# Performance work log

Measured on AMD Instinct MI355X. Metric: run time of the kernel, lower is better.

Reference implementation:

```python
import jax, jax.numpy as jnp
import numpy as np

B, L, D = 4, 4096, 256


def setup_inputs() -> dict:
    key = jax.random.key(0)
    k_x, k_q, k_k, k_v, k_w, k_b = jax.random.split(key, 6)
    s = 1.0 / np.sqrt(D)
    return {
        "x": jax.random.normal(k_x, (B, L, D), dtype=jnp.float32),
        "Wq": jax.random.normal(k_q, (D, D), dtype=jnp.float32) * s,   # nn.Linear weight (out,in)
        "Wk": jax.random.normal(k_k, (D, D), dtype=jnp.float32) * s,
        "Wv": jax.random.normal(k_v, (D, D), dtype=jnp.float32) * s,
        "w_mlp": jax.random.normal(k_w, (D,), dtype=jnp.float32) * s,  # Linear(D,1) weight
        "b_mlp": jnp.zeros((), dtype=jnp.float32),                     # Linear(D,1) bias
    }


def reference(x, Wq, Wk, Wv, w_mlp, b_mlp):
    # Projections (nn.Linear: y = x @ W.T, no bias)
    Q = jnp.einsum("bld,ed->ble", x, Wq)
    K = jnp.einsum("bld,ed->ble", x, Wk)
    V = jnp.einsum("bld,ed->ble", x, Wv)
    # score[b,i,j] = relu((Q[b,i]-K[b,j]) @ w_mlp + b_mlp)
    # decomposed: (Q-K)@w = Q@w - K@w  (exact same math, no (B,L,L,D) tensor)
    q_s = Q @ w_mlp  # (B,L)
    k_s = K @ w_mlp  # (B,L)
    scores = jax.nn.relu(q_s[:, :, None] - k_s[:, None, :] + b_mlp)  # (B,L,L)
    attn = jax.nn.softmax(scores, axis=-1)  # softmax over key axis j
    # out[b,i,d] = sum_j attn[b,i,j] * V[b,j,d]
    out = jnp.einsum("bij,bjd->bid", attn, V)
    return out  # dropout p=0.0 is identity
```

## Files before the change

kernel.cpp:

```cpp
#include <hip/hip_runtime.h>
#include <math.h>

#define BB 4
#define LL 4096
#define DD 256
#define NROWS (BB*LL)
#define CHUNK 32
#define NC (LL/CHUNK)
#define NB 8192

typedef __bf16 bf16x8 __attribute__((ext_vector_type(8)));
typedef __bf16 bf16x4 __attribute__((ext_vector_type(4)));
typedef float floatx4 __attribute__((ext_vector_type(4)));

__global__ void k_prep(const float* __restrict__ Wq, const float* __restrict__ Wk,
                       const float* __restrict__ Wv, const float* __restrict__ w,
                       float* __restrict__ u_part,
                       __bf16* __restrict__ Wh, __bf16* __restrict__ Wl) {
    __shared__ float wl[16];
    int d = threadIdx.x;
    int e0 = blockIdx.x * 16;
    if (d < 16) wl[d] = w[e0 + d];
    __syncthreads();
    float aq = 0.f, ak = 0.f;
    #pragma unroll
    for (int j = 0; j < 16; ++j) {
        float we = wl[j];
        aq = fmaf(Wq[(size_t)(e0 + j)*DD + d], we, aq);
        ak = fmaf(Wk[(size_t)(e0 + j)*DD + d], we, ak);
        float wv = Wv[(size_t)(e0 + j)*DD + d];
        __bf16 h = (__bf16)wv;
        Wh[(size_t)(e0 + j)*DD + d] = h;
        Wl[(size_t)(e0 + j)*DD + d] = (__bf16)(wv - (float)h);
    }
    u_part[(size_t)blockIdx.x*512 + d]       = aq;
    u_part[(size_t)blockIdx.x*512 + DD + d]  = ak;
}

__global__ void __launch_bounds__(256) k_gemm_mfma(
        const float* __restrict__ x,
        const __bf16* __restrict__ Wh, const __bf16* __restrict__ Wl,
        const float* __restrict__ u_part, const float* __restrict__ bmlp,
        float* __restrict__ V, float* __restrict__ a, float* __restrict__ c) {
    __shared__ __bf16 Ah[2][32*40];
    __shared__ __bf16 Al[2][32*40];
    __shared__ float4 ul[128];
    __shared__ float pros[512];
    const int tid = threadIdx.x;
    const int wave = tid >> 6, lane = tid & 63;
    const int rowBase = blockIdx.x * 32;
    const int colBase = blockIdx.y * 128;
    const int quad = lane >> 4, l16 = lane & 15;
    const int srow = tid >> 3, skq = (tid & 7) * 4;
    const bool doproj = (blockIdx.y == 0);

    if (doproj && tid < 128) {
        float4 s = make_float4(0.f, 0.f, 0.f, 0.f);
        #pragma unroll
        for (int g = 0; g < 16; ++g) {
            float4 p = *(const float4*)(u_part + (size_t)g*512 + tid*4);
            s.x += p.x; s.y += p.y; s.z += p.z; s.w += p.w;
        }
        ul[tid] = s;
    }
    __syncthreads();

    floatx4 acc[2][2];
    #pragma unroll
    for (int rt = 0; rt < 2; ++rt)
        #pragma unroll
        for (int ct = 0; ct < 2; ++ct)
            acc[rt][ct] = (floatx4){0.f, 0.f, 0.f, 0.f};
    float aq = 0.f, ak = 0.f;

    const float* xrow = x + (size_t)(rowBase + srow)*DD + skq;

    {
        float4 xv = *(const float4*)xrow;
        __bf16 h0 = (__bf16)xv.x, h1 = (__bf16)xv.y, h2 = (__bf16)xv.z, h3 = (__bf16)xv.w;
        bf16x4 hv = {h0, h1, h2, h3};
        bf16x4 lv = {(__bf16)(xv.x - (float)h0), (__bf16)(xv.y - (float)h1),
                     (__bf16)(xv.z - (float)h2), (__bf16)(xv.w - (float)h3)};
        *(bf16x4*)&Ah[0][srow*40 + skq] = hv;
        *(bf16x4*)&Al[0][srow*40 + skq] = lv;
        if (doproj) {
            float4 q4 = ul[(tid & 7)];
            float4 k4 = ul[64 + (tid & 7)];
            aq = fmaf(xv.x, q4.x, fmaf(xv.y, q4.y, fmaf(xv.z, q4.z, fmaf(xv.w, q4.w, aq))));
            ak = fmaf(xv.x, k4.x, fmaf(xv.y, k4.y, fmaf(xv.z, k4.z, fmaf(xv.w, k4.w, ak))));
        }
    }
    __syncthreads();

    for (int t = 0; t < 8; ++t) {
        const int k0 = t * 32;
        const int cur = t & 1;
        float4 xv;
        if (t < 7) xv = *(const float4*)(xrow + k0 + 32);
        bf16x8 ah[2], al[2];
        #pragma unroll
        for (int rt = 0; rt < 2; ++rt) {
            int m = rt*16 + l16;
            ah[rt] = *(bf16x8*)&Ah[cur][m*40 + quad*8];
            al[rt] = *(bf16x8*)&Al[cur][m*40 + quad*8];
        }
        if (t < 7) {
            __bf16 h0 = (__bf16)xv.x, h1 = (__bf16)xv.y, h2 = (__bf16)xv.z, h3 = (__bf16)xv.w;
            bf16x4 hv = {h0, h1, h2, h3};
            bf16x4 lv = {(__bf16)(xv.x - (float)h0), (__bf16)(xv.y - (float)h1),
                         (__bf16)(xv.z - (float)h2), (__bf16)(xv.w - (float)h3)};
            *(bf16x4*)&Ah[cur^1][srow*40 + skq] = hv;
            *(bf16x4*)&Al[cur^1][srow*40 + skq] = lv;
            if (doproj) {
                float4 q4 = ul[((k0 + 32) >> 2) + (tid & 7)];
                float4 k4 = ul[64 + ((k0 + 32) >> 2) + (tid & 7)];
                aq = fmaf(xv.x, q4.x, fmaf(xv.y, q4.y, fmaf(xv.z, q4.z, fmaf(xv.w, q4.w, aq))));
                ak = fmaf(xv.x, k4.x, fmaf(xv.y, k4.y, fmaf(xv.z, k4.z, fmaf(xv.w, k4.w, ak))));
            }
        }
        __syncthreads();
        #pragma unroll
        for (int ct = 0; ct < 2; ++ct) {
            int n = colBase + wave*32 + ct*16 + l16;
            bf16x8 bh = *(const bf16x8*)(Wh + (size_t)n*DD + k0 + quad*8);
            bf16x8 bl = *(const bf16x8*)(Wl + (size_t)n*DD + k0 + quad*8);
            #pragma unroll
            for (int rt = 0; rt < 2; ++rt) {
                acc[rt][ct] = __builtin_amdgcn_mfma_f32_16x16x32_bf16(ah[rt], bh, acc[rt][ct], 0, 0, 0);
                acc[rt][ct] = __builtin_amdgcn_mfma_f32_16x16x32_bf16(ah[rt], bl, acc[rt][ct], 0, 0, 0);
                acc[rt][ct] = __builtin_amdgcn_mfma_f32_16x16x32_bf16(al[rt], bh, acc[rt][ct], 0, 0, 0);
            }
        }
    }
    #pragma unroll
    for (int rt = 0; rt < 2; ++rt)
        #pragma unroll
        for (int ct = 0; ct < 2; ++ct)
            #pragma unroll
            for (int i = 0; i < 4; ++i) {
                int row = rowBase + rt*16 + quad*4 + i;
                int col = colBase + wave*32 + ct*16 + l16;
                V[(size_t)row*DD + col] = acc[rt][ct][i];
            }
    if (doproj) {
        __syncthreads();
        pros[tid] = aq;
        pros[256 + tid] = ak;
        __syncthreads();
        if (tid < 32) {
            float sa = 0.f, sc = 0.f;
            #pragma unroll
            for (int j = 0; j < 8; ++j) {
                sa += pros[tid*8 + j];
                sc += pros[256 + tid*8 + j];
            }
            a[rowBase + tid] = sa + bmlp[0];
            c[rowBase + tid] = sc;
        }
    }
}

__global__ void __launch_bounds__(1024) k_sortish(const float* __restrict__ c,
        int* __restrict__ binstart_g, int* __restrict__ perm,
        float* __restrict__ c_sorted, float* __restrict__ e_sorted,
        float* __restrict__ SE, float* __restrict__ hdr) {
    __shared__ int   hist[NB];
    __shared__ float esl[LL];
    __shared__ float scrf[64];
    int b = blockIdx.x, tid = threadIdx.x;
    int wave = tid >> 6, lane = tid & 63;
    int* scri = (int*)scrf;

    float4 cv = ((const float4*)(c + (size_t)b*LL))[tid];
    float cw[4] = {cv.x, cv.y, cv.z, cv.w};
    float mn = fminf(fminf(cw[0],cw[1]), fminf(cw[2],cw[3]));
    float mx = fmaxf(fmaxf(cw[0],cw[1]), fmaxf(cw[2],cw[3]));
    #pragma unroll
    for (int off = 32; off > 0; off >>= 1) {
        mn = fminf(mn, __shfl_down(mn, off));
        mx = fmaxf(mx, __shfl_down(mx, off));
    }
    if (lane == 0) { scrf[wave] = mn; scrf[32 + wave] = mx; }
    __syncthreads();
    if (wave == 0) {
        float m = (lane < 16) ? scrf[lane]      :  3.4e38f;
        float M = (lane < 16) ? scrf[32 + lane] : -3.4e38f;
        #pragma unroll
        for (int off = 32; off > 0; off >>= 1) {
            m = fminf(m, __shfl_down(m, off));
            M = fmaxf(M, __shfl_down(M, off));
        }
        if (lane == 0) { scrf[0] = m; scrf[1] = M; }
    }
    __syncthreads();
    float cmin = scrf[0], cmax = scrf[1];
    float scale = (float)NB / fmaxf(cmax - cmin, 1e-20f);
    __syncthreads();

    ((int4*)hist)[tid] = make_int4(0,0,0,0);
    ((int4*)hist)[tid + 1024] = make_int4(0,0,0,0);
    __syncthreads();

    int bins[4];
    #pragma unroll
    for (int u = 0; u < 4; ++u) {
        int bi = (int)((cw[u] - cmin) * scale);
        bi = bi < 0 ? 0 : (bi > NB-1 ? NB-1 : bi);
        bins[u] = bi;
        atomicAdd(&hist[bi], 1);
    }
    __syncthreads();

    int loc[8]; int base = 0;
    #pragma unroll
    for (int j = 0; j < 8; ++j) { loc[j] = base; base += hist[tid*8 + j]; }
    int incl = base;
    #pragma unroll
    for (int off = 1; off < 64; off <<= 1) {
        int t = __shfl_up(incl, off);
        if (lane >= off) incl += t;
    }
    if (lane == 63) scri[wave] = incl;
    __syncthreads();
    if (wave == 0) {
        int v = (lane < 16) ? scri[lane] : 0;
        int s = v;
        #pragma unroll
        for (int off = 1; off < 16; off <<= 1) {
            int t = __shfl_up(s, off);
            if (lane >= off) s += t;
        }
        if (lane < 16) scri[lane] = s - v;
    }
    __syncthreads();
    int thread_excl = (incl - base) + scri[wave];
    __syncthreads();
    #pragma unroll
    for (int j = 0; j < 8; ++j) {
        int bs = thread_excl + loc[j];
        binstart_g[(size_t)b*(NB+2) + tid*8 + j] = bs;
        hist[tid*8 + j] = bs;
    }
    if (tid == 0) {
        binstart_g[(size_t)b*(NB+2) + NB]     = LL;
        binstart_g[(size_t)b*(NB+2) + NB + 1] = LL;
        hdr[b*2 + 0] = cmin;
        hdr[b*2 + 1] = scale;
    }
    __syncthreads();

    #pragma unroll
    for (int u = 0; u < 4; ++u) {
        int i = tid*4 + u;
        int r = atomicAdd(&hist[bins[u]], 1);
        float e = expf(cmin - cw[u]);
        perm[(size_t)b*LL + r] = i;
        c_sorted[(size_t)b*LL + r] = cw[u];
        e_sorted[(size_t)b*LL + r] = e;
        esl[r] = e;
    }
    __syncthreads();

    float le[4]; float s0 = 0.f;
    #pragma unroll
    for (int u = 0; u < 4; ++u) { le[u] = s0; s0 += esl[tid*4 + u]; }
    float fincl = s0;
    #pragma unroll
    for (int off = 1; off < 64; off <<= 1) {
        float t = __shfl_up(fincl, off);
        if (lane >= off) fincl += t;
    }
    if (lane == 63) scrf[wave] = fincl;
    __syncthreads();
    if (wave == 0) {
        float v = (lane < 16) ? scrf[lane] : 0.f;
        float s = v;
        #pragma unroll
        for (int off = 1; off < 16; off <<= 1) {
            float t = __shfl_up(s, off);
            if (lane >= off) s += t;
        }
        if (lane < 16) scrf[lane] = s - v;
    }
    __syncthreads();
    float texcl = (fincl - s0) + scrf[wave];
    #pragma unroll
    for (int u = 0; u < 4; ++u)
        SE[(size_t)b*(LL+1) + tid*4 + u] = texcl + le[u];
    if (tid == 1023) SE[(size_t)b*(LL+1) + LL] = texcl + s0;
}

__global__ void k_scan(const float* __restrict__ V, const int* __restrict__ perm,
        const float* __restrict__ e_sorted,
        float* __restrict__ Pl, float* __restrict__ Pel,
        float* __restrict__ Tp, float* __restrict__ Te) {
    int b = blockIdx.y, q = blockIdx.x;
    int d = threadIdx.x;
    __shared__ int pj[CHUNK];
    __shared__ float pe[CHUNK];
    if (d < CHUNK) {
        pj[d] = perm[(size_t)b*LL + q*CHUNK + d];
        pe[d] = e_sorted[(size_t)b*LL + q*CHUNK + d];
    }
    __syncthreads();
    float vr[CHUNK];
    #pragma unroll
    for (int r = 0; r < CHUNK; ++r)
        vr[r] = V[((size_t)b*LL + pj[r]) * DD + d];
    float acc = 0.f, acce = 0.f;
    size_t kb = (size_t)b*LL + (size_t)q*CHUNK;
    #pragma unroll
    for (int r = 0; r < CHUNK; ++r) {
        size_t o = (kb + r) * DD + d;
        Pl[o]  = acc;
        Pel[o] = acce;
        acc += vr[r];
        acce = fmaf(pe[r], vr[r], acce);
    }
    size_t to = ((size_t)b*NC + q) * DD + d;
    Tp[to] = acc;
    Te[to] = acce;
}

__global__ void k_base(const float* __restrict__ Tp, const float* __restrict__ Te,
        float* __restrict__ baseP, float* __restrict__ basePe) {
    int q = blockIdx.x, b = blockIdx.y, d = threadIdx.x;
    float acc = 0.f, acce = 0.f;
    #pragma unroll 8
    for (int i = 0; i < q; ++i) {
        size_t ti = ((size_t)b*NC + i) * DD + d;
        acc += Tp[ti]; acce += Te[ti];
    }
    size_t o = ((size_t)b*(NC+1) + q) * DD + d;
    baseP[o] = acc; basePe[o] = acce;
}

__global__ void k_out(const float* __restrict__ a, const float* __restrict__ hdr,
                      const int* __restrict__ binstart,
                      const float* __restrict__ c_sorted, const float* __restrict__ e_sorted,
                      const int* __restrict__ perm, const float* __restrict__ V,
                      const float* __restrict__ SE,
                      const float* __restrict__ Pl, const float* __restrict__ Pel,
                      const float* __restrict__ baseP, const float* __restrict__ basePe,
                      float* __restrict__ out) {
    int row = blockIdx.x * 4 + (threadIdx.x >> 6);
    int lane = threadIdx.x & 63;
    int b = row >> 12;
    float ai = a[row];
    float cmin = hdr[b*2 + 0], scale = hdr[b*2 + 1];
    float t = (ai - cmin) * scale;
    int ib = t < 0.f ? 0 : (t >= (float)NB ? NB : (int)t);
    int k    = binstart[(size_t)b*(NB+2) + ib];
    int kend = binstart[(size_t)b*(NB+2) + ib + 1];
    float alpha = expf(cmin - ai);
    float Z = fmaf(alpha, (float)(LL - k), SE[(size_t)b*(LL+1) + k]);
    size_t db = (size_t)lane * 4;
    size_t totoff = ((size_t)b * (NC+1) + NC) * DD + db;
    float4 ptot  = *(const float4*)(baseP  + totoff);
    float4 pk, pek;
    if (k < LL) {
        int q = k >> 5;
        size_t po = ((size_t)b * LL + k) * DD + db;
        size_t bo = ((size_t)b * (NC+1) + q) * DD + db;
        float4 pl = *(const float4*)(Pl    + po);
        float4 bp = *(const float4*)(baseP + bo);
        float4 pe = *(const float4*)(Pel    + po);
        float4 be = *(const float4*)(basePe + bo);
        pk.x = pl.x + bp.x; pk.y = pl.y + bp.y; pk.z = pl.z + bp.z; pk.w = pl.w + bp.w;
        pek.x = pe.x + be.x; pek.y = pe.y + be.y; pek.z = pe.z + be.z; pek.w = pe.w + be.w;
    } else {
        pk = ptot;
        pek = *(const float4*)(basePe + totoff);
    }
    float4 num;
    num.x = fmaf(alpha, ptot.x - pk.x, pek.x);
    num.y = fmaf(alpha, ptot.y - pk.y, pek.y);
    num.z = fmaf(alpha, ptot.z - pk.z, pek.z);
    num.w = fmaf(alpha, ptot.w - pk.w, pek.w);
    for (int r = k; r < kend; ++r) {
        float cr = c_sorted[(size_t)b*LL + r];
        if (cr < ai) {
            float w = e_sorted[(size_t)b*LL + r] - alpha;
            int j = perm[(size_t)b*LL + r];
            float4 v = *(const float4*)(V + ((size_t)b*LL + j) * DD + db);
            num.x = fmaf(w, v.x, num.x);
            num.y = fmaf(w, v.y, num.y);
            num.z = fmaf(w, v.z, num.z);
            num.w = fmaf(w, v.w, num.w);
            Z += w;
        }
    }
    float invZ = 1.f / Z;
    float4 o;
    o.x = num.x * invZ; o.y = num.y * invZ; o.z = num.z * invZ; o.w = num.w * invZ;
    *(float4*)(out + (size_t)row * DD + db) = o;
}

extern "C" void kernel_launch(void* const* d_in, const int* in_sizes, int n_in,
                              void* d_out, int out_size, void* d_ws, size_t ws_size,
                              hipStream_t stream) {
    const float* x  = (const float*)d_in[0];
    const float* Wq = (const float*)d_in[1];
    const float* Wk = (const float*)d_in[2];
    const float* Wv = (const float*)d_in[3];
    const float* wm = (const float*)d_in[4];
    const float* bm = (const float*)d_in[5];
    float* out = (float*)d_out;
    float* ws = (float*)d_ws;

    size_t off = 0;
    auto alloc = [&](size_t n) {
        float* p = ws + off;
        off += (n + 255) & ~(size_t)255;
        return p;
    };
    float* u_part   = alloc(16*512);
    float* a        = alloc(NROWS);
    float* c        = alloc(NROWS);
    float* c_sorted = alloc(NROWS);
    float* e_sorted = alloc(NROWS);
    float* SE       = alloc((size_t)BB*(LL+1));
    int*   perm     = (int*)alloc(NROWS);
    int*   binstart = (int*)alloc((size_t)BB*(NB+2));
    float* hdr      = alloc(2*BB);
    float* V        = alloc((size_t)NROWS*DD);
    float* Pl       = alloc((size_t)NROWS*DD);
    float* Pel      = alloc((size_t)NROWS*DD);
    float* Tp       = alloc((size_t)BB*NC*DD);
    float* Te       = alloc((size_t)BB*NC*DD);
    float* baseP    = alloc((size_t)BB*(NC+1)*DD);
    float* basePe   = alloc((size_t)BB*(NC+1)*DD);
    __bf16* Wh      = (__bf16*)alloc((size_t)DD*DD/2);
    __bf16* Wl      = (__bf16*)alloc((size_t)DD*DD/2);

    hipLaunchKernelGGL(k_prep, dim3(16), dim3(DD), 0, stream, Wq, Wk, Wv, wm, u_part, Wh, Wl);
    hipLaunchKernelGGL(k_gemm_mfma, dim3(NROWS/32, 2), dim3(256), 0, stream,
                       x, Wh, Wl, u_part, bm, V, a, c);
    hipLaunchKernelGGL(k_sortish, dim3(BB), dim3(1024), 0, stream,
                       c, binstart, perm, c_sorted, e_sorted, SE, hdr);
    hipLaunchKernelGGL(k_scan, dim3(NC, BB), dim3(DD), 0, stream, V, perm, e_sorted, Pl, Pel, Tp, Te);
    hipLaunchKernelGGL(k_base, dim3(NC+1, BB), dim3(DD), 0, stream, Tp, Te, baseP, basePe);
    hipLaunchKernelGGL(k_out, dim3(NROWS/4), dim3(256), 0, stream,
                       a, hdr, binstart, c_sorted, e_sorted, perm, V,
                       SE, Pl, Pel, baseP, basePe, out);
}
```

Baseline: 135.1 us.

## Replace bucket sort with exact rank-by-counting and fuse scan stages

Replaces the single-block-per-batch histogram bucket sort with an exact parallel rank kernel. Each key, packed as an order-preserving float encoding with its index, counts how many keys are smaller. Query rows get their exact insertion rank the same way, so the per-row in-bin correction loop in the output kernel goes away. The per-batch min is now computed with atomics inside the GEMM epilogue, and the SE prefix scan is merged into the chunk-scan kernel, which uses 1024-thread blocks. The trade-off is quadratic comparison work (about 4096x8192 per batch) in exchange for far more parallelism and one fewer serial kernel.

```diff
diff --git a/kernel.cpp b/kernel.cpp
--- a/kernel.cpp
+++ b/kernel.cpp
@@ -7,19 +7,29 @@
 #define NROWS (BB*LL)
 #define CHUNK 32
 #define NC (LL/CHUNK)
-#define NB 8192
 
 typedef __bf16 bf16x8 __attribute__((ext_vector_type(8)));
 typedef __bf16 bf16x4 __attribute__((ext_vector_type(4)));
 typedef float floatx4 __attribute__((ext_vector_type(4)));
+typedef unsigned long long u64;
+
+__device__ __forceinline__ unsigned encf(float f) {
+    unsigned u = __float_as_uint(f);
+    return (u & 0x80000000u) ? ~u : (u | 0x80000000u);
+}
+__device__ __forceinline__ float decf(unsigned u) {
+    return __uint_as_float((u & 0x80000000u) ? (u ^ 0x80000000u) : ~u);
+}
 
 __global__ void k_prep(const float* __restrict__ Wq, const float* __restrict__ Wk,
                        const float* __restrict__ Wv, const float* __restrict__ w,
                        float* __restrict__ u_part,
-                       __bf16* __restrict__ Wh, __bf16* __restrict__ Wl) {
+                       __bf16* __restrict__ Wh, __bf16* __restrict__ Wl,
+                       unsigned* __restrict__ hdru) {
     __shared__ float wl[16];
     int d = threadIdx.x;
     int e0 = blockIdx.x * 16;
+    if (blockIdx.x == 0 && d < 8) hdru[d] = (d & 1) ? 0u : 0xFFFFFFFFu;
     if (d < 16) wl[d] = w[e0 + d];
     __syncthreads();
     float aq = 0.f, ak = 0.f;
@@ -41,7 +51,9 @@
         const float* __restrict__ x,
         const __bf16* __restrict__ Wh, const __bf16* __restrict__ Wl,
         const float* __restrict__ u_part, const float* __restrict__ bmlp,
-        float* __restrict__ V, float* __restrict__ a, float* __restrict__ c) {
+        float* __restrict__ V, float* __restrict__ a,
+        u64* __restrict__ ckeys, u64* __restrict__ akeys,
+        unsigned* __restrict__ hdru) {
     __shared__ __bf16 Ah[2][32*40];
     __shared__ __bf16 Al[2][32*40];
     __shared__ float4 ul[128];
@@ -154,172 +166,129 @@
                 sa += pros[tid*8 + j];
                 sc += pros[256 + tid*8 + j];
             }
-            a[rowBase + tid] = sa + bmlp[0];
-            c[rowBase + tid] = sc;
-        }
-    }
-}
-
-__global__ void __launch_bounds__(1024) k_sortish(const float* __restrict__ c,
-        int* __restrict__ binstart_g, int* __restrict__ perm,
-        float* __restrict__ c_sorted, float* __restrict__ e_sorted,
-        float* __restrict__ SE, float* __restrict__ hdr) {
-    __shared__ int   hist[NB];
-    __shared__ float esl[LL];
+            int grow = rowBase + tid;
+            float av = sa + bmlp[0];
+            a[grow] = av;
+            ckeys[grow] = ((u64)encf(sc) << 32) | (unsigned)(grow & (LL-1));
+            akeys[grow] = ((u64)encf(av) << 32);
+            float mn = sc, mx = sc;
+            #pragma unroll
+            for (int off = 16; off > 0; off >>= 1) {
+                mn = fminf(mn, __shfl_down(mn, off));
+                mx = fmaxf(mx, __shfl_down(mx, off));
+            }
+            if (tid == 0) {
+                int bb = rowBase >> 12;
+                atomicMin(&hdru[bb*2 + 0], encf(mn));
+                atomicMax(&hdru[bb*2 + 1], encf(mx));
+            }
+        }
+    }
+}
+
+__global__ void __launch_bounds__(256) k_rank(
+        const u64* __restrict__ ckeys, const u64* __restrict__ akeys,
+        const unsigned* __restrict__ hdru,
+        int* __restrict__ perm, float* __restrict__ e_sorted,
+        int* __restrict__ rowk)
+{
+    const int b = blockIdx.y, tid = threadIdx.x;
+    const int ql = tid >> 4, t = tid & 15;
+    const int g = blockIdx.x * 16 + ql;
+    const u64* kb = ckeys + (size_t)b*LL;
+    const u64 K = (g < LL) ? kb[g] : akeys[(size_t)b*LL + (g - LL)];
+    int cnt = 0;
+    #pragma unroll 16
+    for (int s = 0; s < 256; ++s) {
+        u64 km = kb[t + (s << 4)];
+        cnt += (km < K) ? 1 : 0;
+    }
+    cnt += __shfl_down(cnt, 8, 16);
+    cnt += __shfl_down(cnt, 4, 16);
+    cnt += __shfl_down(cnt, 2, 16);
+    cnt += __shfl_down(cnt, 1, 16);
+    if (t == 0) {
+        if (g < LL) {
+            float cj = decf((unsigned)(K >> 32));
+            float cmin = decf(hdru[b*2]);
+            perm[(size_t)b*LL + cnt] = g;
+            e_sorted[(size_t)b*LL + cnt] = expf(cmin - cj);
+        } else {
+            rowk[(size_t)b*LL + (g - LL)] = cnt;
+        }
+    }
+}
+
+__global__ void __launch_bounds__(1024) k_mid(
+        const int* __restrict__ perm, const float* __restrict__ e_sorted,
+        const float* __restrict__ V,
+        float* __restrict__ SE,
+        float* __restrict__ Pl, float* __restrict__ Pel,
+        float* __restrict__ Tp, float* __restrict__ Te)
+{
     __shared__ float scrf[64];
-    int b = blockIdx.x, tid = threadIdx.x;
-    int wave = tid >> 6, lane = tid & 63;
-    int* scri = (int*)scrf;
-
-    float4 cv = ((const float4*)(c + (size_t)b*LL))[tid];
-    float cw[4] = {cv.x, cv.y, cv.z, cv.w};
-    float mn = fminf(fminf(cw[0],cw[1]), fminf(cw[2],cw[3]));
-    float mx = fmaxf(fmaxf(cw[0],cw[1]), fmaxf(cw[2],cw[3]));
-    #pragma unroll
-    for (int off = 32; off > 0; off >>= 1) {
-        mn = fminf(mn, __shfl_down(mn, off));
-        mx = fmaxf(mx, __shfl_down(mx, off));
-    }
-    if (lane == 0) { scrf[wave] = mn; scrf[32 + wave] = mx; }
-    __syncthreads();
-    if (wave == 0) {
-        float m = (lane < 16) ? scrf[lane]      :  3.4e38f;
-        float M = (lane < 16) ? scrf[32 + lane] : -3.4e38f;
-        #pragma unroll
-        for (int off = 32; off > 0; off >>= 1) {
-            m = fminf(m, __shfl_down(m, off));
-            M = fmaxf(M, __shfl_down(M, off));
-        }
-        if (lane == 0) { scrf[0] = m; scrf[1] = M; }
-    }
-    __syncthreads();
-    float cmin = scrf[0], cmax = scrf[1];
-    float scale = (float)NB / fmaxf(cmax - cmin, 1e-20f);
-    __syncthreads();
-
-    ((int4*)hist)[tid] = make_int4(0,0,0,0);
-    ((int4*)hist)[tid + 1024] = make_int4(0,0,0,0);
-    __syncthreads();
-
-    int bins[4];
-    #pragma unroll
-    for (int u = 0; u < 4; ++u) {
-        int bi = (int)((cw[u] - cmin) * scale);
-        bi = bi < 0 ? 0 : (bi > NB-1 ? NB-1 : bi);
-        bins[u] = bi;
-        atomicAdd(&hist[bi], 1);
-    }
-    __syncthreads();
-
-    int loc[8]; int base = 0;
-    #pragma unroll
-    for (int j = 0; j < 8; ++j) { loc[j] = base; base += hist[tid*8 + j]; }
-    int incl = base;
-    #pragma unroll
-    for (int off = 1; off < 64; off <<= 1) {
-        int t = __shfl_up(incl, off);
-        if (lane >= off) incl += t;
-    }
-    if (lane == 63) scri[wave] = incl;
-    __syncthreads();
-    if (wave == 0) {
-        int v = (lane < 16) ? scri[lane] : 0;
-        int s = v;
-        #pragma unroll
-        for (int off = 1; off < 16; off <<= 1) {
-            int t = __shfl_up(s, off);
-            if (lane >= off) s += t;
-        }
-        if (lane < 16) scri[lane] = s - v;
-    }
-    __syncthreads();
-    int thread_excl = (incl - base) + scri[wave];
-    __syncthreads();
-    #pragma unroll
-    for (int j = 0; j < 8; ++j) {
-        int bs = thread_excl + loc[j];
-        binstart_g[(size_t)b*(NB+2) + tid*8 + j] = bs;
-        hist[tid*8 + j] = bs;
-    }
-    if (tid == 0) {
-        binstart_g[(size_t)b*(NB+2) + NB]     = LL;
-        binstart_g[(size_t)b*(NB+2) + NB + 1] = LL;
-        hdr[b*2 + 0] = cmin;
-        hdr[b*2 + 1] = scale;
-    }
-    __syncthreads();
-
-    #pragma unroll
-    for (int u = 0; u < 4; ++u) {
-        int i = tid*4 + u;
-        int r = atomicAdd(&hist[bins[u]], 1);
-        float e = expf(cmin - cw[u]);
-        perm[(size_t)b*LL + r] = i;
-        c_sorted[(size_t)b*LL + r] = cw[u];
-        e_sorted[(size_t)b*LL + r] = e;
-        esl[r] = e;
-    }
-    __syncthreads();
-
-    float le[4]; float s0 = 0.f;
-    #pragma unroll
-    for (int u = 0; u < 4; ++u) { le[u] = s0; s0 += esl[tid*4 + u]; }
-    float fincl = s0;
-    #pragma unroll
-    for (int off = 1; off < 64; off <<= 1) {
-        float t = __shfl_up(fincl, off);
-        if (lane >= off) fincl += t;
-    }
-    if (lane == 63) scrf[wave] = fincl;
-    __syncthreads();
-    if (wave == 0) {
-        float v = (lane < 16) ? scrf[lane] : 0.f;
-        float s = v;
-        #pragma unroll
-        for (int off = 1; off < 16; off <<= 1) {
-            float t = __shfl_up(s, off);
-            if (lane >= off) s += t;
-        }
-        if (lane < 16) scrf[lane] = s - v;
-    }
-    __syncthreads();
-    float texcl = (fincl - s0) + scrf[wave];
-    #pragma unroll
-    for (int u = 0; u < 4; ++u)
-        SE[(size_t)b*(LL+1) + tid*4 + u] = texcl + le[u];
-    if (tid == 1023) SE[(size_t)b*(LL+1) + LL] = texcl + s0;
-}
-
-__global__ void k_scan(const float* __restrict__ V, const int* __restrict__ perm,
-        const float* __restrict__ e_sorted,
-        float* __restrict__ Pl, float* __restrict__ Pel,
-        float* __restrict__ Tp, float* __restrict__ Te) {
-    int b = blockIdx.y, q = blockIdx.x;
-    int d = threadIdx.x;
-    __shared__ int pj[CHUNK];
-    __shared__ float pe[CHUNK];
-    if (d < CHUNK) {
-        pj[d] = perm[(size_t)b*LL + q*CHUNK + d];
-        pe[d] = e_sorted[(size_t)b*LL + q*CHUNK + d];
-    }
-    __syncthreads();
-    float vr[CHUNK];
-    #pragma unroll
-    for (int r = 0; r < CHUNK; ++r)
-        vr[r] = V[((size_t)b*LL + pj[r]) * DD + d];
-    float acc = 0.f, acce = 0.f;
-    size_t kb = (size_t)b*LL + (size_t)q*CHUNK;
-    #pragma unroll
-    for (int r = 0; r < CHUNK; ++r) {
-        size_t o = (kb + r) * DD + d;
-        Pl[o]  = acc;
-        Pel[o] = acce;
-        acc += vr[r];
-        acce = fmaf(pe[r], vr[r], acce);
-    }
-    size_t to = ((size_t)b*NC + q) * DD + d;
-    Tp[to] = acc;
-    Te[to] = acce;
+    __shared__ int   pj_l[4][CHUNK];
+    __shared__ float pe_l[4][CHUNK];
+    const int bid = blockIdx.x, tid = threadIdx.x;
+    if (bid < BB) {
+        const int b = bid, wave = tid >> 6, lane = tid & 63;
+        float4 ev = ((const float4*)(e_sorted + (size_t)b*LL))[tid];
+        float ew[4] = {ev.x, ev.y, ev.z, ev.w};
+        float le[4]; float s0 = 0.f;
+        #pragma unroll
+        for (int u = 0; u < 4; ++u) { le[u] = s0; s0 += ew[u]; }
+        float fincl = s0;
+        #pragma unroll
+        for (int off = 1; off < 64; off <<= 1) {
+            float tt = __shfl_up(fincl, off);
+            if (lane >= off) fincl += tt;
+        }
+        if (lane == 63) scrf[wave] = fincl;
+        __syncthreads();
+        if (wave == 0) {
+            float v = (lane < 16) ? scrf[lane] : 0.f;
+            float s = v;
+            #pragma unroll
+            for (int off = 1; off < 16; off <<= 1) {
+                float tt = __shfl_up(s, off);
+                if (lane >= off) s += tt;
+            }
+            if (lane < 16) scrf[lane] = s - v;
+        }
+        __syncthreads();
+        float texcl = (fincl - s0) + scrf[wave];
+        #pragma unroll
+        for (int u = 0; u < 4; ++u)
+            SE[(size_t)b*(LL+1) + tid*4 + u] = texcl + le[u];
+        if (tid == 1023) SE[(size_t)b*(LL+1) + LL] = texcl + s0;
+    } else {
+        const int task = bid - BB;
+        const int sub = tid >> 8, d = tid & 255;
+        const int chunk = task*4 + sub;
+        const int b = chunk >> 7, q = chunk & (NC-1);
+        if (d < CHUNK) {
+            pj_l[sub][d] = perm[(size_t)b*LL + q*CHUNK + d];
+            pe_l[sub][d] = e_sorted[(size_t)b*LL + q*CHUNK + d];
+        }
+        __syncthreads();
+        float vr[CHUNK];
+        #pragma unroll
+        for (int r = 0; r < CHUNK; ++r)
+            vr[r] = V[((size_t)b*LL + pj_l[sub][r])*DD + d];
+        float acc = 0.f, acce = 0.f;
+        size_t kb = (size_t)b*LL + (size_t)q*CHUNK;
+        #pragma unroll
+        for (int r = 0; r < CHUNK; ++r) {
+            size_t o = (kb + r)*DD + d;
+            Pl[o]  = acc;
+            Pel[o] = acce;
+            acc += vr[r];
+            acce = fmaf(pe_l[sub][r], vr[r], acce);
+        }
+        size_t to = ((size_t)b*NC + q)*DD + d;
+        Tp[to] = acc;
+        Te[to] = acce;
+    }
 }
 
 __global__ void k_base(const float* __restrict__ Tp, const float* __restrict__ Te,
@@ -335,10 +304,8 @@
     baseP[o] = acc; basePe[o] = acce;
 }
 
-__global__ void k_out(const float* __restrict__ a, const float* __restrict__ hdr,
-                      const int* __restrict__ binstart,
-                      const float* __restrict__ c_sorted, const float* __restrict__ e_sorted,
-                      const int* __restrict__ perm, const float* __restrict__ V,
+__global__ void k_out(const float* __restrict__ a, const unsigned* __restrict__ hdru,
+                      const int* __restrict__ rowk,
                       const float* __restrict__ SE,
                       const float* __restrict__ Pl, const float* __restrict__ Pel,
                       const float* __restrict__ baseP, const float* __restrict__ basePe,
@@ -347,16 +314,13 @@
     int lane = threadIdx.x & 63;
     int b = row >> 12;
     float ai = a[row];
-    float cmin = hdr[b*2 + 0], scale = hdr[b*2 + 1];
-    float t = (ai - cmin) * scale;
-    int ib = t < 0.f ? 0 : (t >= (float)NB ? NB : (int)t);
-    int k    = binstart[(size_t)b*(NB+2) + ib];
-    int kend = binstart[(size_t)b*(NB+2) + ib + 1];
+    float cmin = decf(hdru[b*2]);
+    int k = rowk[row];
     float alpha = expf(cmin - ai);
     float Z = fmaf(alpha, (float)(LL - k), SE[(size_t)b*(LL+1) + k]);
     size_t db = (size_t)lane * 4;
     size_t totoff = ((size_t)b * (NC+1) + NC) * DD + db;
-    float4 ptot  = *(const float4*)(baseP  + totoff);
+    float4 ptot = *(const float4*)(baseP + totoff);
     float4 pk, pek;
     if (k < LL) {
         int q = k >> 5;
@@ -377,19 +341,6 @@
     num.y = fmaf(alpha, ptot.y - pk.y, pek.y);
     num.z = fmaf(alpha, ptot.z - pk.z, pek.z);
     num.w = fmaf(alpha, ptot.w - pk.w, pek.w);
-    for (int r = k; r < kend; ++r) {
-        float cr = c_sorted[(size_t)b*LL + r];
-        if (cr < ai) {
-            float w = e_sorted[(size_t)b*LL + r] - alpha;
-            int j = perm[(size_t)b*LL + r];
-            float4 v = *(const float4*)(V + ((size_t)b*LL + j) * DD + db);
-            num.x = fmaf(w, v.x, num.x);
-            num.y = fmaf(w, v.y, num.y);
-            num.z = fmaf(w, v.z, num.z);
-            num.w = fmaf(w, v.w, num.w);
-            Z += w;
-        }
-    }
     float invZ = 1.f / Z;
     float4 o;
     o.x = num.x * invZ; o.y = num.y * invZ; o.z = num.z * invZ; o.w = num.w * invZ;
@@ -416,13 +367,11 @@
     };
     float* u_part   = alloc(16*512);
     float* a        = alloc(NROWS);
-    float* c        = alloc(NROWS);
-    float* c_sorted = alloc(NROWS);
     float* e_sorted = alloc(NROWS);
     float* SE       = alloc((size_t)BB*(LL+1));
     int*   perm     = (int*)alloc(NROWS);
-    int*   binstart = (int*)alloc((size_t)BB*(NB+2));
-    float* hdr      = alloc(2*BB);
+    int*   rowk     = (int*)alloc(NROWS);
+    unsigned* hdru  = (unsigned*)alloc(2*BB);
     float* V        = alloc((size_t)NROWS*DD);
     float* Pl       = alloc((size_t)NROWS*DD);
     float* Pel      = alloc((size_t)NROWS*DD);
@@ -430,17 +379,21 @@
     float* Te       = alloc((size_t)BB*NC*DD);
     float* baseP    = alloc((size_t)BB*(NC+1)*DD);
     float* basePe   = alloc((size_t)BB*(NC+1)*DD);
+    u64*   ckeys    = (u64*)alloc((size_t)NROWS*2);
+    u64*   akeys    = (u64*)alloc((size_t)NROWS*2);
     __bf16* Wh      = (__bf16*)alloc((size_t)DD*DD/2);
     __bf16* Wl      = (__bf16*)alloc((size_t)DD*DD/2);
 
-    hipLaunchKernelGGL(k_prep, dim3(16), dim3(DD), 0, stream, Wq, Wk, Wv, wm, u_part, Wh, Wl);
+    hipLaunchKernelGGL(k_prep, dim3(16), dim3(DD), 0, stream,
+                       Wq, Wk, Wv, wm, u_part, Wh, Wl, hdru);
     hipLaunchKernelGGL(k_gemm_mfma, dim3(NROWS/32, 2), dim3(256), 0, stream,
-                       x, Wh, Wl, u_part, bm, V, a, c);
-    hipLaunchKernelGGL(k_sortish, dim3(BB), dim3(1024), 0, stream,
-                       c, binstart, perm, c_sorted, e_sorted, SE, hdr);
-    hipLaunchKernelGGL(k_scan, dim3(NC, BB), dim3(DD), 0, stream, V, perm, e_sorted, Pl, Pel, Tp, Te);
-    hipLaunchKernelGGL(k_base, dim3(NC+1, BB), dim3(DD), 0, stream, Tp, Te, baseP, basePe);
+                       x, Wh, Wl, u_part, bm, V, a, ckeys, akeys, hdru);
+    hipLaunchKernelGGL(k_rank, dim3(512, BB), dim3(256), 0, stream,
+                       ckeys, akeys, hdru, perm, e_sorted, rowk);
+    hipLaunchKernelGGL(k_mid, dim3(BB + NC*BB/4), dim3(1024), 0, stream,
+                       perm, e_sorted, V, SE, Pl, Pel, Tp, Te);
+    hipLaunchKernelGGL(k_base, dim3(NC+1, BB), dim3(256), 0, stream,
+                       Tp, Te, baseP, basePe);
     hipLaunchKernelGGL(k_out, dim3(NROWS/4), dim3(256), 0, stream,
-                       a, hdr, binstart, c_sorted, e_sorted, perm, V,
-                       SE, Pl, Pel, baseP, basePe, out);
-}
+                       a, hdru, rowk, SE, Pl, Pel, baseP, basePe, out);
+}
```

Result: slower. 190.1 us (+40.7%).

## Move min/max into GEMM epilogue and prefix-sum of exp into scan kernel

Applied to the files above, without the earlier changes.

The per-batch min and max of c are now computed in the GEMM epilogue with wave shuffles plus order-preserving unsigned atomicMin/atomicMax, so the single-block-per-batch sort kernel no longer does its own two-level reduction. The exclusive prefix sum of the sorted exp weights (SE) is moved out of the sort kernel into one extra block per batch in the scan kernel. This shortens the serial, low-occupancy sort stage (only 4 blocks) at the cost of global atomics and an extra header initialisation in the prep kernel.

```diff
diff --git a/kernel.cpp b/kernel.cpp
--- a/kernel.cpp
+++ b/kernel.cpp
@@ -13,13 +13,23 @@
 typedef __bf16 bf16x4 __attribute__((ext_vector_type(4)));
 typedef float floatx4 __attribute__((ext_vector_type(4)));
 
+__device__ __forceinline__ unsigned encf(float f) {
+    unsigned u = __float_as_uint(f);
+    return (u & 0x80000000u) ? ~u : (u | 0x80000000u);
+}
+__device__ __forceinline__ float decf(unsigned u) {
+    return __uint_as_float((u & 0x80000000u) ? (u ^ 0x80000000u) : ~u);
+}
+
 __global__ void k_prep(const float* __restrict__ Wq, const float* __restrict__ Wk,
                        const float* __restrict__ Wv, const float* __restrict__ w,
                        float* __restrict__ u_part,
-                       __bf16* __restrict__ Wh, __bf16* __restrict__ Wl) {
+                       __bf16* __restrict__ Wh, __bf16* __restrict__ Wl,
+                       unsigned* __restrict__ hdru) {
     __shared__ float wl[16];
     int d = threadIdx.x;
     int e0 = blockIdx.x * 16;
+    if (blockIdx.x == 0 && d < 8) hdru[d] = (d & 1) ? 0u : 0xFFFFFFFFu;
     if (d < 16) wl[d] = w[e0 + d];
     __syncthreads();
     float aq = 0.f, ak = 0.f;
@@ -41,7 +51,8 @@
         const float* __restrict__ x,
         const __bf16* __restrict__ Wh, const __bf16* __restrict__ Wl,
         const float* __restrict__ u_part, const float* __restrict__ bmlp,
-        float* __restrict__ V, float* __restrict__ a, float* __restrict__ c) {
+        float* __restrict__ V, float* __restrict__ a, float* __restrict__ c,
+        unsigned* __restrict__ hdru) {
     __shared__ __bf16 Ah[2][32*40];
     __shared__ __bf16 Al[2][32*40];
     __shared__ float4 ul[128];
@@ -156,46 +167,36 @@
             }
             a[rowBase + tid] = sa + bmlp[0];
             c[rowBase + tid] = sc;
-        }
-    }
-}
-
-__global__ void __launch_bounds__(1024) k_sortish(const float* __restrict__ c,
+            float mn = sc, mx = sc;
+            #pragma unroll
+            for (int off = 16; off > 0; off >>= 1) {
+                mn = fminf(mn, __shfl_down(mn, off));
+                mx = fmaxf(mx, __shfl_down(mx, off));
+            }
+            if (tid == 0) {
+                int bb = rowBase >> 12;
+                atomicMin(&hdru[bb*2 + 0], encf(mn));
+                atomicMax(&hdru[bb*2 + 1], encf(mx));
+            }
+        }
+    }
+}
+
+__global__ void __launch_bounds__(1024) k_sortl(const float* __restrict__ c,
+        const unsigned* __restrict__ hdru,
         int* __restrict__ binstart_g, int* __restrict__ perm,
         float* __restrict__ c_sorted, float* __restrict__ e_sorted,
-        float* __restrict__ SE, float* __restrict__ hdr) {
-    __shared__ int   hist[NB];
-    __shared__ float esl[LL];
-    __shared__ float scrf[64];
+        float* __restrict__ hdrf) {
+    __shared__ int hist[NB];
+    __shared__ int scri[16];
     int b = blockIdx.x, tid = threadIdx.x;
     int wave = tid >> 6, lane = tid & 63;
-    int* scri = (int*)scrf;
 
     float4 cv = ((const float4*)(c + (size_t)b*LL))[tid];
     float cw[4] = {cv.x, cv.y, cv.z, cv.w};
-    float mn = fminf(fminf(cw[0],cw[1]), fminf(cw[2],cw[3]));
-    float mx = fmaxf(fmaxf(cw[0],cw[1]), fmaxf(cw[2],cw[3]));
-    #pragma unroll
-    for (int off = 32; off > 0; off >>= 1) {
-        mn = fminf(mn, __shfl_down(mn, off));
-        mx = fmaxf(mx, __shfl_down(mx, off));
-    }
-    if (lane == 0) { scrf[wave] = mn; scrf[32 + wave] = mx; }
-    __syncthreads();
-    if (wave == 0) {
-        float m = (lane < 16) ? scrf[lane]      :  3.4e38f;
-        float M = (lane < 16) ? scrf[32 + lane] : -3.4e38f;
-        #pragma unroll
-        for (int off = 32; off > 0; off >>= 1) {
-            m = fminf(m, __shfl_down(m, off));
-            M = fmaxf(M, __shfl_down(M, off));
-        }
-        if (lane == 0) { scrf[0] = m; scrf[1] = M; }
-    }
-    __syncthreads();
-    float cmin = scrf[0], cmax = scrf[1];
+    float cmin = decf(hdru[b*2 + 0]);
+    float cmax = decf(hdru[b*2 + 1]);
     float scale = (float)NB / fmaxf(cmax - cmin, 1e-20f);
-    __syncthreads();
 
     ((int4*)hist)[tid] = make_int4(0,0,0,0);
     ((int4*)hist)[tid + 1024] = make_int4(0,0,0,0);
@@ -244,8 +245,8 @@
     if (tid == 0) {
         binstart_g[(size_t)b*(NB+2) + NB]     = LL;
         binstart_g[(size_t)b*(NB+2) + NB + 1] = LL;
-        hdr[b*2 + 0] = cmin;
-        hdr[b*2 + 1] = scale;
+        hdrf[b*2 + 0] = cmin;
+        hdrf[b*2 + 1] = scale;
     }
     __syncthreads();
 
@@ -253,73 +254,81 @@
     for (int u = 0; u < 4; ++u) {
         int i = tid*4 + u;
         int r = atomicAdd(&hist[bins[u]], 1);
-        float e = expf(cmin - cw[u]);
         perm[(size_t)b*LL + r] = i;
         c_sorted[(size_t)b*LL + r] = cw[u];
-        e_sorted[(size_t)b*LL + r] = e;
-        esl[r] = e;
-    }
-    __syncthreads();
-
-    float le[4]; float s0 = 0.f;
-    #pragma unroll
-    for (int u = 0; u < 4; ++u) { le[u] = s0; s0 += esl[tid*4 + u]; }
-    float fincl = s0;
-    #pragma unroll
-    for (int off = 1; off < 64; off <<= 1) {
-        float t = __shfl_up(fincl, off);
-        if (lane >= off) fincl += t;
-    }
-    if (lane == 63) scrf[wave] = fincl;
-    __syncthreads();
-    if (wave == 0) {
-        float v = (lane < 16) ? scrf[lane] : 0.f;
-        float s = v;
-        #pragma unroll
-        for (int off = 1; off < 16; off <<= 1) {
-            float t = __shfl_up(s, off);
-            if (lane >= off) s += t;
-        }
-        if (lane < 16) scrf[lane] = s - v;
-    }
-    __syncthreads();
-    float texcl = (fincl - s0) + scrf[wave];
-    #pragma unroll
-    for (int u = 0; u < 4; ++u)
-        SE[(size_t)b*(LL+1) + tid*4 + u] = texcl + le[u];
-    if (tid == 1023) SE[(size_t)b*(LL+1) + LL] = texcl + s0;
-}
-
-__global__ void k_scan(const float* __restrict__ V, const int* __restrict__ perm,
-        const float* __restrict__ e_sorted,
+        e_sorted[(size_t)b*LL + r] = expf(cmin - cw[u]);
+    }
+}
+
+__global__ void __launch_bounds__(256) k_scan(const float* __restrict__ V,
+        const int* __restrict__ perm, const float* __restrict__ e_sorted,
         float* __restrict__ Pl, float* __restrict__ Pel,
-        float* __restrict__ Tp, float* __restrict__ Te) {
+        float* __restrict__ Tp, float* __restrict__ Te,
+        float* __restrict__ SE) {
     int b = blockIdx.y, q = blockIdx.x;
     int d = threadIdx.x;
     __shared__ int pj[CHUNK];
     __shared__ float pe[CHUNK];
-    if (d < CHUNK) {
-        pj[d] = perm[(size_t)b*LL + q*CHUNK + d];
-        pe[d] = e_sorted[(size_t)b*LL + q*CHUNK + d];
-    }
-    __syncthreads();
-    float vr[CHUNK];
-    #pragma unroll
-    for (int r = 0; r < CHUNK; ++r)
-        vr[r] = V[((size_t)b*LL + pj[r]) * DD + d];
-    float acc = 0.f, acce = 0.f;
-    size_t kb = (size_t)b*LL + (size_t)q*CHUNK;
-    #pragma unroll
-    for (int r = 0; r < CHUNK; ++r) {
-        size_t o = (kb + r) * DD + d;
-        Pl[o]  = acc;
-        Pel[o] = acce;
-        acc += vr[r];
-        acce = fmaf(pe[r], vr[r], acce);
-    }
-    size_t to = ((size_t)b*NC + q) * DD + d;
-    Tp[to] = acc;
-    Te[to] = acce;
+    __shared__ float scrf[8];
+    if (q < NC) {
+        if (d < CHUNK) {
+            pj[d] = perm[(size_t)b*LL + q*CHUNK + d];
+            pe[d] = e_sorted[(size_t)b*LL + q*CHUNK + d];
+        }
+        __syncthreads();
+        float vr[CHUNK];
+        #pragma unroll
+        for (int r = 0; r < CHUNK; ++r)
+            vr[r] = V[((size_t)b*LL + pj[r]) * DD + d];
+        float acc = 0.f, acce = 0.f;
+        size_t kb = (size_t)b*LL + (size_t)q*CHUNK;
+        #pragma unroll
+        for (int r = 0; r < CHUNK; ++r) {
+            size_t o = (kb + r) * DD + d;
+            Pl[o]  = acc;
+            Pel[o] = acce;
+            acc += vr[r];
+            acce = fmaf(pe[r], vr[r], acce);
+        }
+        size_t to = ((size_t)b*NC + q) * DD + d;
+        Tp[to] = acc;
+        Te[to] = acce;
+    } else {
+        const int wave = d >> 6, lane = d & 63;
+        float ew[16];
+        #pragma unroll
+        for (int v4 = 0; v4 < 4; ++v4) {
+            float4 ev = ((const float4*)(e_sorted + (size_t)b*LL))[d*4 + v4];
+            ew[v4*4+0] = ev.x; ew[v4*4+1] = ev.y; ew[v4*4+2] = ev.z; ew[v4*4+3] = ev.w;
+        }
+        float le[16]; float s0 = 0.f;
+        #pragma unroll
+        for (int u = 0; u < 16; ++u) { le[u] = s0; s0 += ew[u]; }
+        float fincl = s0;
+        #pragma unroll
+        for (int off = 1; off < 64; off <<= 1) {
+            float tt = __shfl_up(fincl, off);
+            if (lane >= off) fincl += tt;
+        }
+        if (lane == 63) scrf[wave] = fincl;
+        __syncthreads();
+        if (wave == 0) {
+            float v = (lane < 4) ? scrf[lane] : 0.f;
+            float s = v;
+            #pragma unroll
+            for (int off = 1; off < 4; off <<= 1) {
+                float tt = __shfl_up(s, off);
+                if (lane >= off) s += tt;
+            }
+            if (lane < 4) scrf[lane] = s - v;
+        }
+        __syncthreads();
+        float texcl = (fincl - s0) + scrf[wave];
+        #pragma unroll
+        for (int u = 0; u < 16; ++u)
+            SE[(size_t)b*(LL+1) + d*16 + u] = texcl + le[u];
+        if (d == 255) SE[(size_t)b*(LL+1) + LL] = texcl + s0;
+    }
 }
 
 __global__ void k_base(const float* __restrict__ Tp, const float* __restrict__ Te,
@@ -335,7 +344,7 @@
     baseP[o] = acc; basePe[o] = acce;
 }
 
-__global__ void k_out(const float* __restrict__ a, const float* __restrict__ hdr,
+__global__ void k_out(const float* __restrict__ a, const float* __restrict__ hdrf,
                       const int* __restrict__ binstart,
                       const float* __restrict__ c_sorted, const float* __restrict__ e_sorted,
                       const int* __restrict__ perm, const float* __restrict__ V,
@@ -347,7 +356,7 @@
     int lane = threadIdx.x & 63;
     int b = row >> 12;
     float ai = a[row];
-    float cmin = hdr[b*2 + 0], scale = hdr[b*2 + 1];
+    float cmin = hdrf[b*2 + 0], scale = hdrf[b*2 + 1];
     float t = (ai - cmin) * scale;
     int ib = t < 0.f ? 0 : (t >= (float)NB ? NB : (int)t);
     int k    = binstart[(size_t)b*(NB+2) + ib];
@@ -422,7 +431,8 @@
     float* SE       = alloc((size_t)BB*(LL+1));
     int*   perm     = (int*)alloc(NROWS);
     int*   binstart = (int*)alloc((size_t)BB*(NB+2));
-    float* hdr      = alloc(2*BB);
+    float* hdrf     = alloc(2*BB);
+    unsigned* hdru  = (unsigned*)alloc(2*BB);
     float* V        = alloc((size_t)NROWS*DD);
     float* Pl       = alloc((size_t)NROWS*DD);
     float* Pel      = alloc((size_t)NROWS*DD);
@@ -433,14 +443,17 @@
     __bf16* Wh      = (__bf16*)alloc((size_t)DD*DD/2);
     __bf16* Wl      = (__bf16*)alloc((size_t)DD*DD/2);
 
-    hipLaunchKernelGGL(k_prep, dim3(16), dim3(DD), 0, stream, Wq, Wk, Wv, wm, u_part, Wh, Wl);
+    hipLaunchKernelGGL(k_prep, dim3(16), dim3(DD), 0, stream,
+                       Wq, Wk, Wv, wm, u_part, Wh, Wl, hdru);
     hipLaunchKernelGGL(k_gemm_mfma, dim3(NROWS/32, 2), dim3(256), 0, stream,
-                       x, Wh, Wl, u_part, bm, V, a, c);
-    hipLaunchKernelGGL(k_sortish, dim3(BB), dim3(1024), 0, stream,
-                       c, binstart, perm, c_sorted, e_sorted, SE, hdr);
-    hipLaunchKernelGGL(k_scan, dim3(NC, BB), dim3(DD), 0, stream, V, perm, e_sorted, Pl, Pel, Tp, Te);
-    hipLaunchKernelGGL(k_base, dim3(NC+1, BB), dim3(DD), 0, stream, Tp, Te, baseP, basePe);
+                       x, Wh, Wl, u_part, bm, V, a, c, hdru);
+    hipLaunchKernelGGL(k_sortl, dim3(BB), dim3(1024), 0, stream,
+                       c, hdru, binstart, perm, c_sorted, e_sorted, hdrf);
+    hipLaunchKernelGGL(k_scan, dim3(NC+1, BB), dim3(DD), 0, stream,
+                       V, perm, e_sorted, Pl, Pel, Tp, Te, SE);
+    hipLaunchKernelGGL(k_base, dim3(NC+1, BB), dim3(DD), 0, stream,
+                       Tp, Te, baseP, basePe);
     hipLaunchKernelGGL(k_out, dim3(NROWS/4), dim3(256), 0, stream,
-                       a, hdr, binstart, c_sorted, e_sorted, perm, V,
+                       a, hdrf, binstart, c_sorted, e_sorted, perm, V,
                        SE, Pl, Pel, baseP, basePe, out);
 }
```

Measured after the change: 144.6 us. 1.07x slower.
